# Optimization experiments

Hardware: AMD Instinct MI355X
Metric: run time of the kernel (lower is better)

Reference implementation:

```python
import jax, jax.numpy as jnp
import numpy as np

EPS = 1e-8  # torch.cosine_similarity default eps


def setup_inputs() -> dict:
    key = jax.random.key(0)
    ks = jax.random.split(key, 6)
    B, S, H, D = 512, 4096, 32, 16
    return {
        "decoder_hidden_final_layer": jax.random.normal(ks[0], (B, H), dtype=jnp.float32),
        "encoder_outputs": jax.random.normal(ks[1], (B, S, H), dtype=jnp.float32),
        "Wq": jax.random.normal(ks[2], (D, H), dtype=jnp.float32) * 0.1,
        "bq": jax.random.normal(ks[3], (D,), dtype=jnp.float32) * 0.1,
        "Wk": jax.random.normal(ks[4], (D, H), dtype=jnp.float32) * 0.1,
        "bk": jax.random.normal(ks[5], (D,), dtype=jnp.float32) * 0.1,
    }


def reference(decoder_hidden_final_layer, encoder_outputs, Wq, bq, Wk, bk):
    # q projection of encoder outputs: [B,S,D]; k projection of decoder state: [B,D]
    q = jnp.einsum("bsh,dh->bsd", encoder_outputs, Wq) + bq
    k = decoder_hidden_final_layer @ Wk.T + bk
    # cosine similarity: normalize once, then a single contraction (same math as
    # torch.cosine_similarity with eps clamp on the norms)
    qn = q / jnp.maximum(jnp.linalg.norm(q, axis=-1, keepdims=True), EPS)
    kn = k / jnp.maximum(jnp.linalg.norm(k, axis=-1, keepdims=True), EPS)
    attention = jnp.einsum("bsd,bd->bs", qn, kn)  # [B,S]
    weightings = jax.nn.log_softmax(attention, axis=1)  # softmax over S (torch dim=1)
    return weightings[:, None, :]  # transpose(1,2): [B,1,S]
```

## Files before the change

kernel.cpp:

```cpp
#include <hip/hip_runtime.h>
#include <math.h>

#define BB     512
#define SS     4096
#define HH     32
#define DD     16
#define CHUNK  256
#define NCH    (SS / CHUNK)
#define STRIDE 33
#define NT     256
#define EPSI   1e-8f

__global__ __launch_bounds__(NT, 2)
void attn_cos_logsoftmax(const float* __restrict__ dec,
                         const float* __restrict__ enc,
                         const float* __restrict__ Wq,
                         const float* __restrict__ bq,
                         const float* __restrict__ Wk,
                         const float* __restrict__ bk,
                         float* __restrict__ out)
{
    __shared__ float wqT[HH * DD];
    __shared__ float buf[CHUNK * STRIDE];
    __shared__ float red[8];

    const int t = threadIdx.x;
    const int b = blockIdx.x;

    for (int e = t; e < DD * HH; e += NT) {
        int d = e >> 5;
        int h = e & 31;
        wqT[h * DD + d] = Wq[e];
    }

    float bqr[DD];
#pragma unroll
    for (int d = 0; d < DD; ++d) bqr[d] = bq[d];

    float kn[DD];
    {
        float dh[HH];
#pragma unroll
        for (int h = 0; h < HH; ++h) dh[h] = dec[b * HH + h];
        float ss = 0.f;
#pragma unroll
        for (int d = 0; d < DD; ++d) {
            float a = bk[d];
#pragma unroll
            for (int h = 0; h < HH; ++h) a = fmaf(Wk[d * HH + h], dh[h], a);
            kn[d] = a;
            ss = fmaf(a, a, ss);
        }
        float inv = 1.f / fmaxf(sqrtf(ss), EPSI);
#pragma unroll
        for (int d = 0; d < DD; ++d) kn[d] *= inv;
    }

    const float4* encb = (const float4*)(enc + (size_t)b * SS * HH);

    float4 pf[8];
#pragma unroll
    for (int i = 0; i < 8; ++i) pf[i] = encb[i * NT + t];

    __syncthreads();

    float att[NCH];

    for (int c = 0; c < NCH; ++c) {
#pragma unroll
        for (int i = 0; i < 8; ++i) {
            int idx = i * NT + t;
            int row = idx >> 3;
            int c4  = idx & 7;
            float* p = &buf[row * STRIDE + c4 * 4];
            p[0] = pf[i].x; p[1] = pf[i].y; p[2] = pf[i].z; p[3] = pf[i].w;
        }
        __syncthreads();

        if (c + 1 < NCH) {
            const float4* src = encb + (size_t)(c + 1) * (CHUNK * HH / 4);
#pragma unroll
            for (int i = 0; i < 8; ++i) pf[i] = src[i * NT + t];
        }

        float q[DD];
#pragma unroll
        for (int d = 0; d < DD; ++d) q[d] = bqr[d];
        const float* hrow = &buf[t * STRIDE];
#pragma unroll
        for (int h = 0; h < HH; ++h) {
            float hv = hrow[h];
            const float* w = &wqT[h * DD];
#pragma unroll
            for (int d = 0; d < DD; ++d) q[d] = fmaf(w[d], hv, q[d]);
        }
        float ss = 0.f, num = 0.f;
#pragma unroll
        for (int d = 0; d < DD; ++d) {
            ss  = fmaf(q[d], q[d], ss);
            num = fmaf(q[d], kn[d], num);
        }
        att[c] = num / fmaxf(sqrtf(ss), EPSI);

        __syncthreads();
    }

    float m = -INFINITY;
#pragma unroll
    for (int c = 0; c < NCH; ++c) m = fmaxf(m, att[c]);
#pragma unroll
    for (int off = 32; off >= 1; off >>= 1) m = fmaxf(m, __shfl_down(m, off));
    const int wave = t >> 6;
    if ((t & 63) == 0) red[wave] = m;
    __syncthreads();
    m = fmaxf(fmaxf(red[0], red[1]), fmaxf(red[2], red[3]));

    float sum = 0.f;
#pragma unroll
    for (int c = 0; c < NCH; ++c) sum += __expf(att[c] - m);
#pragma unroll
    for (int off = 32; off >= 1; off >>= 1) sum += __shfl_down(sum, off);
    if ((t & 63) == 0) red[4 + wave] = sum;
    __syncthreads();
    sum = (red[4] + red[5]) + (red[6] + red[7]);

    const float logZ = m + __logf(sum);

    float* ob = out + (size_t)b * SS;
#pragma unroll
    for (int c = 0; c < NCH; ++c) ob[c * CHUNK + t] = att[c] - logZ;
}

extern "C" void kernel_launch(void* const* d_in, const int* in_sizes, int n_in,
                              void* d_out, int out_size, void* d_ws, size_t ws_size,
                              hipStream_t stream) {
    const float* dec = (const float*)d_in[0];
    const float* enc = (const float*)d_in[1];
    const float* Wq  = (const float*)d_in[2];
    const float* bq  = (const float*)d_in[3];
    const float* Wk  = (const float*)d_in[4];
    const float* bk  = (const float*)d_in[5];
    float* out = (float*)d_out;

    attn_cos_logsoftmax<<<dim3(BB), dim3(NT), 0, stream>>>(dec, enc, Wq, bq, Wk, bk, out);
}
```

Baseline: 383.9 us.

## Load encoder rows directly into registers with 1024-thread blocks, drop LDS staging

Each thread now reads its own 32-float encoder row straight from global memory into a double-buffered register array, replacing the shared-memory transpose staging and its per-chunk barriers. The block grows to 1024 threads, each handling 4 rows, and Wq is read through uniform scalar loads instead of an LDS-transposed copy. This removes LDS traffic and synchronisation but makes global loads per-thread strided by 128 bytes, so accesses are less coalesced. It also raises register pressure and may limit occupancy.

```diff
diff --git a/kernel.cpp b/kernel.cpp
--- a/kernel.cpp
+++ b/kernel.cpp
@@ -1,17 +1,15 @@
 #include <hip/hip_runtime.h>
 #include <math.h>
 
-#define BB     512
-#define SS     4096
-#define HH     32
-#define DD     16
-#define CHUNK  256
-#define NCH    (SS / CHUNK)
-#define STRIDE 33
-#define NT     256
-#define EPSI   1e-8f
+#define BB   512
+#define SS   4096
+#define HH   32
+#define DD   16
+#define NT   1024
+#define RPT  (SS / NT)
+#define EPSI 1e-8f
 
-__global__ __launch_bounds__(NT, 2)
+__global__ __launch_bounds__(NT, 4)
 void attn_cos_logsoftmax(const float* __restrict__ dec,
                          const float* __restrict__ enc,
                          const float* __restrict__ Wq,
@@ -20,115 +18,126 @@
                          const float* __restrict__ bk,
                          float* __restrict__ out)
 {
-    __shared__ float wqT[HH * DD];
-    __shared__ float buf[CHUNK * STRIDE];
-    __shared__ float red[8];
+    __shared__ float knS[DD];
+    __shared__ float red1[16];
+    __shared__ float red2[16];
 
     const int t = threadIdx.x;
     const int b = blockIdx.x;
 
-    for (int e = t; e < DD * HH; e += NT) {
-        int d = e >> 5;
-        int h = e & 31;
-        wqT[h * DD + d] = Wq[e];
+    const float* encb = enc + (size_t)b * SS * HH;
+
+    float hbuf[2][HH];
+    {
+        const float4* p = (const float4*)(encb + (size_t)t * HH);
+#pragma unroll
+        for (int i = 0; i < 8; ++i) {
+            float4 v = p[i];
+            hbuf[0][i * 4 + 0] = v.x;
+            hbuf[0][i * 4 + 1] = v.y;
+            hbuf[0][i * 4 + 2] = v.z;
+            hbuf[0][i * 4 + 3] = v.w;
+        }
     }
 
-    float bqr[DD];
-#pragma unroll
-    for (int d = 0; d < DD; ++d) bqr[d] = bq[d];
-
-    float kn[DD];
     {
         float dh[HH];
 #pragma unroll
         for (int h = 0; h < HH; ++h) dh[h] = dec[b * HH + h];
-        float ss = 0.f;
+        float kacc[DD];
+        float ssk = 0.f;
 #pragma unroll
         for (int d = 0; d < DD; ++d) {
             float a = bk[d];
 #pragma unroll
             for (int h = 0; h < HH; ++h) a = fmaf(Wk[d * HH + h], dh[h], a);
-            kn[d] = a;
-            ss = fmaf(a, a, ss);
+            kacc[d] = a;
+            ssk = fmaf(a, a, ssk);
         }
-        float inv = 1.f / fmaxf(sqrtf(ss), EPSI);
+        float inv = 1.f / fmaxf(sqrtf(ssk), EPSI);
+        if (t == 0) {
 #pragma unroll
-        for (int d = 0; d < DD; ++d) kn[d] *= inv;
+            for (int d = 0; d < DD; ++d) knS[d] = kacc[d] * inv;
+        }
     }
-
-    const float4* encb = (const float4*)(enc + (size_t)b * SS * HH);
-
-    float4 pf[8];
-#pragma unroll
-    for (int i = 0; i < 8; ++i) pf[i] = encb[i * NT + t];
-
     __syncthreads();
 
-    float att[NCH];
+    float att[RPT];
 
-    for (int c = 0; c < NCH; ++c) {
 #pragma unroll
-        for (int i = 0; i < 8; ++i) {
-            int idx = i * NT + t;
-            int row = idx >> 3;
-            int c4  = idx & 7;
-            float* p = &buf[row * STRIDE + c4 * 4];
-            p[0] = pf[i].x; p[1] = pf[i].y; p[2] = pf[i].z; p[3] = pf[i].w;
-        }
-        __syncthreads();
+    for (int c = 0; c < RPT; ++c) {
+        const int cur = c & 1;
+        const int nxt = cur ^ 1;
 
-        if (c + 1 < NCH) {
-            const float4* src = encb + (size_t)(c + 1) * (CHUNK * HH / 4);
+        if (c + 1 < RPT) {
+            const float4* p =
+                (const float4*)(encb + (size_t)((c + 1) * NT + t) * HH);
 #pragma unroll
-            for (int i = 0; i < 8; ++i) pf[i] = src[i * NT + t];
+            for (int i = 0; i < 8; ++i) {
+                float4 v = p[i];
+                hbuf[nxt][i * 4 + 0] = v.x;
+                hbuf[nxt][i * 4 + 1] = v.y;
+                hbuf[nxt][i * 4 + 2] = v.z;
+                hbuf[nxt][i * 4 + 3] = v.w;
+            }
         }
 
         float q[DD];
 #pragma unroll
-        for (int d = 0; d < DD; ++d) q[d] = bqr[d];
-        const float* hrow = &buf[t * STRIDE];
+        for (int d = 0; d < DD; ++d) q[d] = bq[d];
 #pragma unroll
         for (int h = 0; h < HH; ++h) {
-            float hv = hrow[h];
-            const float* w = &wqT[h * DD];
+            float hv = hbuf[cur][h];
 #pragma unroll
-            for (int d = 0; d < DD; ++d) q[d] = fmaf(w[d], hv, q[d]);
+            for (int d = 0; d < DD; ++d)
+                q[d] = fmaf(Wq[d * HH + h], hv, q[d]);
         }
+
         float ss = 0.f, num = 0.f;
 #pragma unroll
-        for (int d = 0; d < DD; ++d) {
-            ss  = fmaf(q[d], q[d], ss);
-            num = fmaf(q[d], kn[d], num);
+        for (int dd = 0; dd < DD; dd += 4) {
+            float4 k4 = *((const float4*)&knS[dd]);
+            ss  = fmaf(q[dd + 0], q[dd + 0], ss);
+            ss  = fmaf(q[dd + 1], q[dd + 1], ss);
+            ss  = fmaf(q[dd + 2], q[dd + 2], ss);
+            ss  = fmaf(q[dd + 3], q[dd + 3], ss);
+            num = fmaf(q[dd + 0], k4.x, num);
+            num = fmaf(q[dd + 1], k4.y, num);
+            num = fmaf(q[dd + 2], k4.z, num);
+            num = fmaf(q[dd + 3], k4.w, num);
         }
         att[c] = num / fmaxf(sqrtf(ss), EPSI);
-
-        __syncthreads();
     }
 
-    float m = -INFINITY;
+    const int wave = t >> 6;
+
+    float m = att[0];
 #pragma unroll
-    for (int c = 0; c < NCH; ++c) m = fmaxf(m, att[c]);
+    for (int c = 1; c < RPT; ++c) m = fmaxf(m, att[c]);
 #pragma unroll
     for (int off = 32; off >= 1; off >>= 1) m = fmaxf(m, __shfl_down(m, off));
-    const int wave = t >> 6;
-    if ((t & 63) == 0) red[wave] = m;
+    if ((t & 63) == 0) red1[wave] = m;
     __syncthreads();
-    m = fmaxf(fmaxf(red[0], red[1]), fmaxf(red[2], red[3]));
+    float M = red1[0];
+#pragma unroll
+    for (int w = 1; w < 16; ++w) M = fmaxf(M, red1[w]);
 
-    float sum = 0.f;
+    float s = 0.f;
 #pragma unroll
-    for (int c = 0; c < NCH; ++c) sum += __expf(att[c] - m);
+    for (int c = 0; c < RPT; ++c) s += __expf(att[c] - M);
 #pragma unroll
-    for (int off = 32; off >= 1; off >>= 1) sum += __shfl_down(sum, off);
-    if ((t & 63) == 0) red[4 + wave] = sum;
+    for (int off = 32; off >= 1; off >>= 1) s += __shfl_down(s, off);
+    if ((t & 63) == 0) red2[wave] = s;
     __syncthreads();
-    sum = (red[4] + red[5]) + (red[6] + red[7]);
+    float S = 0.f;
+#pragma unroll
+    for (int w = 0; w < 16; ++w) S += red2[w];
 
-    const float logZ = m + __logf(sum);
+    const float logZ = M + __logf(S);
 
     float* ob = out + (size_t)b * SS;
 #pragma unroll
-    for (int c = 0; c < NCH; ++c) ob[c * CHUNK + t] = att[c] - logZ;
+    for (int c = 0; c < RPT; ++c) ob[c * NT + t] = att[c] - logZ;
 }
 
 extern "C" void kernel_launch(void* const* d_in, const int* in_sizes, int n_in,
```

New measurement: 465.2 us. +21.2%, slower.

## Compute Q projection with bf16 MFMA and double-buffered LDS staging

Applied to the files above, without the earlier changes.

Replaces the per-thread scalar FMA projection of encoder rows with a 16x16x32 bf16 MFMA per 16-row tile. Encoder chunks are converted to bf16 into double-buffered shared memory, which removes one barrier per chunk. Row norms and dot products are reduced across lanes with DPP, and attention scores are staged in LDS so the output can be written with float4 stores. This cuts FP32 ALU work on a memory-bound kernel, at the cost of bf16 rounding error in q.

```diff
diff --git a/kernel.cpp b/kernel.cpp
--- a/kernel.cpp
+++ b/kernel.cpp
@@ -1,15 +1,38 @@
 #include <hip/hip_runtime.h>
 #include <math.h>
 
-#define BB     512
-#define SS     4096
-#define HH     32
-#define DD     16
-#define CHUNK  256
-#define NCH    (SS / CHUNK)
-#define STRIDE 33
-#define NT     256
-#define EPSI   1e-8f
+#define BB    512
+#define SS    4096
+#define HH    32
+#define DD    16
+#define NT    256
+#define CHUNK 256
+#define NCH   (SS / CHUNK)
+#define TILES (CHUNK / 16)
+#define TPW   (TILES / 4)
+#define EPSI  1e-8f
+
+typedef __attribute__((ext_vector_type(8))) short   short8;
+typedef __attribute__((ext_vector_type(4))) float   floatx4;
+
+__device__ __forceinline__ short bf16_of(float f) {
+    union { float f; unsigned u; } v; v.f = f;
+    return (short)((v.u + 0x7FFFu + ((v.u >> 16) & 1u)) >> 16);
+}
+
+template <int CTRL>
+__device__ __forceinline__ float dpp_add(float x) {
+    int xi = __builtin_bit_cast(int, x);
+    int yi = __builtin_amdgcn_update_dpp(0, xi, CTRL, 0xF, 0xF, true);
+    return x + __builtin_bit_cast(float, yi);
+}
+__device__ __forceinline__ float red16(float x) {
+    x = dpp_add<0xB1>(x);
+    x = dpp_add<0x4E>(x);
+    x = dpp_add<0x141>(x);
+    x = dpp_add<0x140>(x);
+    return x;
+}
 
 __global__ __launch_bounds__(NT, 2)
 void attn_cos_logsoftmax(const float* __restrict__ dec,
@@ -20,115 +43,123 @@
                          const float* __restrict__ bk,
                          float* __restrict__ out)
 {
-    __shared__ float wqT[HH * DD];
-    __shared__ float buf[CHUNK * STRIDE];
-    __shared__ float red[8];
+    __shared__ short encS[2][CHUNK * HH];
+    __shared__ float attS[SS];
+    __shared__ float knS[DD];
+    __shared__ float redM[4], redS[4];
 
-    const int t = threadIdx.x;
-    const int b = blockIdx.x;
+    const int t    = threadIdx.x;
+    const int b    = blockIdx.x;
+    const int lane = t & 63;
+    const int wv   = t >> 6;
+    const int l15  = lane & 15;
+    const int quad = lane >> 4;
 
-    for (int e = t; e < DD * HH; e += NT) {
-        int d = e >> 5;
-        int h = e & 31;
-        wqT[h * DD + d] = Wq[e];
+    const float4* encb4 = (const float4*)(enc + (size_t)b * SS * HH);
+
+    float4 pf[8];
+#pragma unroll
+    for (int i = 0; i < 8; ++i) pf[i] = encb4[i * NT + t];
+
+    short8 bfrag;
+    {
+        const float* wp = Wq + l15 * HH + quad * 8;
+        float4 w0 = *(const float4*)wp;
+        float4 w1 = *(const float4*)(wp + 4);
+        bfrag[0] = bf16_of(w0.x); bfrag[1] = bf16_of(w0.y);
+        bfrag[2] = bf16_of(w0.z); bfrag[3] = bf16_of(w0.w);
+        bfrag[4] = bf16_of(w1.x); bfrag[5] = bf16_of(w1.y);
+        bfrag[6] = bf16_of(w1.z); bfrag[7] = bf16_of(w1.w);
     }
 
-    float bqr[DD];
-#pragma unroll
-    for (int d = 0; d < DD; ++d) bqr[d] = bq[d];
+    const float bqV = bq[l15];
 
-    float kn[DD];
     {
         float dh[HH];
 #pragma unroll
         for (int h = 0; h < HH; ++h) dh[h] = dec[b * HH + h];
-        float ss = 0.f;
+        float kacc[DD], ssk = 0.f;
 #pragma unroll
         for (int d = 0; d < DD; ++d) {
             float a = bk[d];
 #pragma unroll
             for (int h = 0; h < HH; ++h) a = fmaf(Wk[d * HH + h], dh[h], a);
-            kn[d] = a;
-            ss = fmaf(a, a, ss);
+            kacc[d] = a; ssk = fmaf(a, a, ssk);
         }
-        float inv = 1.f / fmaxf(sqrtf(ss), EPSI);
+        float inv = 1.f / fmaxf(sqrtf(ssk), EPSI);
+        if (t == 0) {
 #pragma unroll
-        for (int d = 0; d < DD; ++d) kn[d] *= inv;
+            for (int d = 0; d < DD; ++d) knS[d] = kacc[d] * inv;
+        }
     }
-
-    const float4* encb = (const float4*)(enc + (size_t)b * SS * HH);
-
-    float4 pf[8];
-#pragma unroll
-    for (int i = 0; i < 8; ++i) pf[i] = encb[i * NT + t];
-
     __syncthreads();
-
-    float att[NCH];
+    const float knV = knS[l15];
 
     for (int c = 0; c < NCH; ++c) {
+        short* dst = encS[c & 1];
 #pragma unroll
         for (int i = 0; i < 8; ++i) {
-            int idx = i * NT + t;
-            int row = idx >> 3;
-            int c4  = idx & 7;
-            float* p = &buf[row * STRIDE + c4 * 4];
-            p[0] = pf[i].x; p[1] = pf[i].y; p[2] = pf[i].z; p[3] = pf[i].w;
+            union { short s[4]; unsigned long long u; } pk;
+            pk.s[0] = bf16_of(pf[i].x); pk.s[1] = bf16_of(pf[i].y);
+            pk.s[2] = bf16_of(pf[i].z); pk.s[3] = bf16_of(pf[i].w);
+            *(unsigned long long*)&dst[(i * NT + t) * 4] = pk.u;
+        }
+        if (c + 1 < NCH) {
+            const float4* src = encb4 + (size_t)(c + 1) * (CHUNK * HH / 4);
+#pragma unroll
+            for (int i = 0; i < 8; ++i) pf[i] = src[i * NT + t];
         }
         __syncthreads();
 
-        if (c + 1 < NCH) {
-            const float4* src = encb + (size_t)(c + 1) * (CHUNK * HH / 4);
+        const short* sbuf = encS[c & 1];
+        const int cbase = c * CHUNK;
 #pragma unroll
-            for (int i = 0; i < 8; ++i) pf[i] = src[i * NT + t];
+        for (int i2 = 0; i2 < TPW; ++i2) {
+            const int tile = wv * TPW + i2;
+            short8 afrag = *(const short8*)&sbuf[(tile * 16 + l15) * HH + quad * 8];
+            floatx4 acc = {0.f, 0.f, 0.f, 0.f};
+            acc = __builtin_amdgcn_mfma_f32_16x16x32_bf16(afrag, bfrag, acc, 0, 0, 0);
+            float4 av;
+            float* avp = &av.x;
+#pragma unroll
+            for (int r = 0; r < 4; ++r) {
+                float qv = acc[r] + bqV;
+                float ss = red16(qv * qv);
+                float nu = red16(qv * knV);
+                avp[r] = nu / fmaxf(sqrtf(ss), EPSI);
+            }
+            if (l15 == 0)
+                *(float4*)&attS[cbase + tile * 16 + quad * 4] = av;
         }
-
-        float q[DD];
-#pragma unroll
-        for (int d = 0; d < DD; ++d) q[d] = bqr[d];
-        const float* hrow = &buf[t * STRIDE];
-#pragma unroll
-        for (int h = 0; h < HH; ++h) {
-            float hv = hrow[h];
-            const float* w = &wqT[h * DD];
-#pragma unroll
-            for (int d = 0; d < DD; ++d) q[d] = fmaf(w[d], hv, q[d]);
-        }
-        float ss = 0.f, num = 0.f;
-#pragma unroll
-        for (int d = 0; d < DD; ++d) {
-            ss  = fmaf(q[d], q[d], ss);
-            num = fmaf(q[d], kn[d], num);
-        }
-        att[c] = num / fmaxf(sqrtf(ss), EPSI);
-
-        __syncthreads();
     }
+    __syncthreads();
 
     float m = -INFINITY;
 #pragma unroll
-    for (int c = 0; c < NCH; ++c) m = fmaxf(m, att[c]);
+    for (int i = 0; i < 16; ++i) m = fmaxf(m, attS[t + i * NT]);
 #pragma unroll
     for (int off = 32; off >= 1; off >>= 1) m = fmaxf(m, __shfl_down(m, off));
-    const int wave = t >> 6;
-    if ((t & 63) == 0) red[wave] = m;
+    if (lane == 0) redM[wv] = m;
     __syncthreads();
-    m = fmaxf(fmaxf(red[0], red[1]), fmaxf(red[2], red[3]));
+    const float M = fmaxf(fmaxf(redM[0], redM[1]), fmaxf(redM[2], redM[3]));
 
-    float sum = 0.f;
+    float s = 0.f;
 #pragma unroll
-    for (int c = 0; c < NCH; ++c) sum += __expf(att[c] - m);
+    for (int i = 0; i < 16; ++i) s += __expf(attS[t + i * NT] - M);
 #pragma unroll
-    for (int off = 32; off >= 1; off >>= 1) sum += __shfl_down(sum, off);
-    if ((t & 63) == 0) red[4 + wave] = sum;
+    for (int off = 32; off >= 1; off >>= 1) s += __shfl_down(s, off);
+    if (lane == 0) redS[wv] = s;
     __syncthreads();
-    sum = (red[4] + red[5]) + (red[6] + red[7]);
+    const float S = (redS[0] + redS[1]) + (redS[2] + redS[3]);
+    const float logZ = M + __logf(S);
 
-    const float logZ = m + __logf(sum);
-
-    float* ob = out + (size_t)b * SS;
+    float4* ob4 = (float4*)(out + (size_t)b * SS);
 #pragma unroll
-    for (int c = 0; c < NCH; ++c) ob[c * CHUNK + t] = att[c] - logZ;
+    for (int i = 0; i < 4; ++i) {
+        float4 a4 = *(const float4*)&attS[(t + i * NT) * 4];
+        a4.x -= logZ; a4.y -= logZ; a4.z -= logZ; a4.w -= logZ;
+        ob4[t + i * NT] = a4;
+    }
 }
 
 extern "C" void kernel_launch(void* const* d_in, const int* in_sizes, int n_in,
```

Result: no change. 379.5 us (-1.1%).
